# Kernel tuning notes

Hardware: AMD Instinct MI355X
Metric: run time of the kernel (lower is better)

The kernel has to match this reference:

```python
import jax, jax.numpy as jnp
from jax import lax
import numpy as np

B, T = 64, 256
V_CHAR, V_DICT = 8000, 30
CHAR_E, POS_E = 256, 128
POS_H, MAIN_H = 256, 512      # bidirectional output dims
LBL = 18 + 2                  # label_size + START/STOP


def _lstm_dir(x, maskf, Wih, Whh, b):
    """Unidirectional LSTM with PyTorch gate order (i,f,g,o); masked steps hold state, outputs zeroed at pads."""
    Bb = x.shape[0]
    H = Whh.shape[1]
    def step(carry, inp):
        h, c = carry
        xt, mt = inp  # xt [B,D], mt [B,1]
        g = xt @ Wih.T + h @ Whh.T + b
        i, f, gg, o = jnp.split(g, 4, axis=-1)
        c2 = jax.nn.sigmoid(f) * c + jax.nn.sigmoid(i) * jnp.tanh(gg)
        h2 = jax.nn.sigmoid(o) * jnp.tanh(c2)
        h = mt * h2 + (1.0 - mt) * h
        c = mt * c2 + (1.0 - mt) * c
        return (h, c), h * mt
    init = (jnp.zeros((Bb, H), x.dtype), jnp.zeros((Bb, H), x.dtype))
    _, ys = lax.scan(step, init, (x.transpose(1, 0, 2), maskf.T[:, :, None]))
    return ys.transpose(1, 0, 2)  # [B,T,H]


def _bilstm(x, lengths, maskf, Wih_f, Whh_f, b_f, Wih_b, Whh_b, b_b):
    """Packed-sequence BiLSTM: backward direction runs over each sequence reversed by its own length."""
    Tt = x.shape[1]
    out_f = _lstm_dir(x, maskf, Wih_f, Whh_f, b_f)
    rev_idx = jnp.clip(lengths[:, None] - 1 - jnp.arange(Tt)[None, :], 0, Tt - 1)  # [B,T]
    x_rev = jnp.take_along_axis(x, rev_idx[:, :, None], axis=1)
    out_b_rev = _lstm_dir(x_rev, maskf, Wih_b, Whh_b, b_b)
    out_b = jnp.take_along_axis(out_b_rev, rev_idx[:, :, None], axis=1) * maskf[:, :, None]
    return jnp.concatenate([out_f, out_b], axis=-1)


def _viterbi(emit, mask, trans):
    """CRF Viterbi decode. emit [B,T,L], mask [B,T] bool, trans [L,L] (trans[i,j]=score i->j); START=L-2, STOP=L-1."""
    Bb, Tt, L = emit.shape
    START, STOP = L - 2, L - 1
    alpha0 = trans[START][None, :] + emit[:, 0]  # [B,L]
    ident = jnp.arange(L)[None, :]
    def step(alpha, inp):
        e_t, m_t = inp  # [B,L], [B,1]
        scores = alpha[:, :, None] + trans[None, :, :]  # [B,L_prev,L_cur]
        bp = jnp.argmax(scores, axis=1)
        new = jnp.max(scores, axis=1) + e_t
        alpha = jnp.where(m_t, new, alpha)
        bp = jnp.where(m_t, bp, ident)
        return alpha, bp
    alpha, bps = lax.scan(step, alpha0, (emit[:, 1:].transpose(1, 0, 2), mask[:, 1:].T[:, :, None]))
    final = alpha + trans[:, STOP][None, :]
    last_tag = jnp.argmax(final, axis=1)          # [B]
    path_score = jnp.max(final, axis=1)           # [B]
    def back(tag, bp_t):
        prev = jnp.take_along_axis(bp_t, tag[:, None], axis=1)[:, 0]
        return prev, tag
    first_tag, tags_rest = lax.scan(back, last_tag, bps, reverse=True)  # tags_rest [T-1,B]
    tags = jnp.concatenate([first_tag[:, None], tags_rest.T], axis=1)   # [B,T]
    return path_score, tags * mask.astype(tags.dtype)


def setup_inputs() -> dict:
    key = jax.random.key(0)
    ks = jax.random.split(key, 24)
    char_inputs = jax.random.randint(ks[0], (B, T), 0, V_CHAR)
    pos_inputs = jax.random.randint(ks[1], (B, T), 0, V_DICT)
    tag_inputs = jax.random.randint(ks[2], (B, T), 0, V_DICT)
    lengths = jnp.sort(jax.random.randint(ks[3], (B,), T // 2, T + 1))[::-1]
    lengths = lengths.at[0].set(T)  # pack_padded requires descending lengths; max len defines T
    mask = jnp.arange(T)[None, :] < lengths[:, None]
    s = 0.08
    def rn(k, shape):
        return jax.random.normal(k, shape, jnp.float32) * s
    Hp, Hm = POS_H // 2, MAIN_H // 2
    Dm = CHAR_E + POS_E + POS_H
    return dict(
        char_inputs=char_inputs, pos_inputs=pos_inputs, tag_inputs=tag_inputs,
        lengths=lengths, mask=mask,
        char_emb=rn(ks[4], (V_CHAR, CHAR_E)),
        pos_emb=rn(ks[5], (V_DICT, POS_E)),
        tag_pos_emb=rn(ks[6], (V_DICT, POS_E)),
        pWih_f=rn(ks[7], (4 * Hp, POS_E)), pWhh_f=rn(ks[8], (4 * Hp, Hp)), pb_f=rn(ks[9], (4 * Hp,)),
        pWih_b=rn(ks[10], (4 * Hp, POS_E)), pWhh_b=rn(ks[11], (4 * Hp, Hp)), pb_b=rn(ks[12], (4 * Hp,)),
        mWih_f=rn(ks[13], (4 * Hm, Dm)), mWhh_f=rn(ks[14], (4 * Hm, Hm)), mb_f=rn(ks[15], (4 * Hm,)),
        mWih_b=rn(ks[16], (4 * Hm, Dm)), mWhh_b=rn(ks[17], (4 * Hm, Hm)), mb_b=rn(ks[18], (4 * Hm,)),
        W_out=rn(ks[19], (LBL, MAIN_H)), b_out=rn(ks[20], (LBL,)),
        trans=rn(ks[21], (LBL, LBL)),
    )


def reference(char_inputs, pos_inputs, tag_inputs, lengths, mask,
              char_emb, pos_emb, tag_pos_emb,
              pWih_f, pWhh_f, pb_f, pWih_b, pWhh_b, pb_b,
              mWih_f, mWhh_f, mb_f, mWih_b, mWhh_b, mb_b,
              W_out, b_out, trans):
    maskf = mask.astype(jnp.float32)
    # PosBiLSTM: embeds tag_inputs with its own pos table, runs BiLSTM (dropout is identity at eval)
    tag_embs = tag_pos_emb[tag_inputs]
    pos_lstm_out = _bilstm(tag_embs, lengths, maskf, pWih_f, pWhh_f, pb_f, pWih_b, pWhh_b, pb_b)
    # Main BiLSTM over [char_emb | pos_emb | pos_lstm_out]
    emb = jnp.concatenate([char_emb[char_inputs], pos_emb[pos_inputs], pos_lstm_out], axis=-1)
    lstm_out = _bilstm(emb, lengths, maskf, mWih_f, mWhh_f, mb_f, mWih_b, mWhh_b, mb_b)
    emit = lstm_out @ W_out.T + b_out  # [B,T,LBL]
    _, tag_seq = _viterbi(emit, mask, trans)
    return tag_seq
```

## Files before the change

### kernel.cpp

```cpp
#include <hip/hip_runtime.h>
#include <hip/hip_bf16.h>
#include <math.h>


#define Bsz 64
#define Tsz 256
#define NROW 16384

__device__ __forceinline__ float sigm(float x) { return 1.f / (1.f + expf(-x)); }

#define PIN4(v) asm volatile("" : "+v"((v).x), "+v"((v).y), "+v"((v).z), "+v"((v).w))

typedef float f32x4 __attribute__((ext_vector_type(4)));
typedef short short8 __attribute__((ext_vector_type(8)));
typedef unsigned short u16;
typedef u16 u16x8 __attribute__((ext_vector_type(8)));

__device__ __forceinline__ void bf16split(float f, u16& h, u16& l) {
  unsigned u = __float_as_uint(f);
  unsigned hh = (u + 0x7FFFu + ((u >> 16) & 1u)) >> 16;
  h = (u16)hh;
  float hf = __uint_as_float(hh << 16);
  unsigned v = __float_as_uint(f - hf);
  l = (u16)((v + 0x7FFFu + ((v >> 16) & 1u)) >> 16);
}

__global__ __launch_bounds__(256) void wsplit4(
    const float* __restrict__ s0, u16* __restrict__ h0, u16* __restrict__ l0, int n0,
    const float* __restrict__ s1, u16* __restrict__ h1, u16* __restrict__ l1, int n1,
    const float* __restrict__ s2, u16* __restrict__ h2, u16* __restrict__ l2, int n2,
    const float* __restrict__ s3, u16* __restrict__ h3, u16* __restrict__ l3, int n3) {
  int i = (blockIdx.x * 256 + threadIdx.x) * 4;
  const float* s; u16 *h, *l;
  if (i < n0) { s = s0; h = h0; l = l0; }
  else if ((i -= n0) < n1) { s = s1; h = h1; l = l1; }
  else if ((i -= n1) < n2) { s = s2; h = h2; l = l2; }
  else if ((i -= n2) < n3) { s = s3; h = h3; l = l3; }
  else return;
  float4 v = *(const float4*)&s[i];
  ushort4 hh, ll;
  bf16split(v.x, hh.x, ll.x); bf16split(v.y, hh.y, ll.y);
  bf16split(v.z, hh.z, ll.z); bf16split(v.w, hh.w, ll.w);
  *(ushort4*)&h[i] = hh; *(ushort4*)&l[i] = ll;
}

__global__ __launch_bounds__(256) void gather_kernel(
    const int* __restrict__ ci, const int* __restrict__ pi, const int* __restrict__ ti,
    const float* __restrict__ ce, const float* __restrict__ pe, const float* __restrict__ te,
    u16* __restrict__ tbh, u16* __restrict__ tbl,
    u16* __restrict__ emh, u16* __restrict__ eml) {
  int gid = blockIdx.x * 256 + threadIdx.x;
  int m = gid >> 7, s = gid & 127;
  float4 v; size_t off; u16 *ph, *pl;
  if (s < 32) {
    v = ((const float4*)&te[(size_t)ti[m] * 128])[s];
    off = (size_t)m * 128 + s * 4; ph = tbh; pl = tbl;
  } else if (s < 96) {
    v = ((const float4*)&ce[(size_t)ci[m] * 256])[s - 32];
    off = (size_t)m * 640 + (s - 32) * 4; ph = emh; pl = eml;
  } else {
    v = ((const float4*)&pe[(size_t)pi[m] * 128])[s - 96];
    off = (size_t)m * 640 + 256 + (s - 96) * 4; ph = emh; pl = eml;
  }
  ushort4 h, l;
  bf16split(v.x, h.x, l.x); bf16split(v.y, h.y, l.y);
  bf16split(v.z, h.z, l.z); bf16split(v.w, h.w, l.w);
  *(ushort4*)&ph[off] = h; *(ushort4*)&pl[off] = l;
}

#define GTM 512
#define GTN 128
__global__ __launch_bounds__(512) void gemm_bf16x3(
    const u16* __restrict__ Ah, const u16* __restrict__ Al,
    const u16* __restrict__ Wh, const u16* __restrict__ Wl,
    const float* __restrict__ biasF, const float* __restrict__ biasB,
    float* __restrict__ C, int ldc, int K, int NhB) {
  extern __shared__ u16 us[];
  u16* As_h = us;
  u16* As_l = us + 512 * 40;
  u16* Ws_h = us + 2 * 512 * 40;
  u16* Ws_l = us + 2 * 512 * 40 + 128 * 40;
  const int tid = threadIdx.x;
  const int lane = tid & 63, wv = tid >> 6;
  const int l15 = lane & 15, l8 = (lane >> 4) * 8, l4 = lane >> 4;
  const int m0 = blockIdx.y * GTM;
  const int n0 = blockIdx.x * GTN;
  const u16* WhS = Wh + (size_t)n0 * K;
  const u16* WlS = Wl + (size_t)n0 * K;
  const float* bias = (blockIdx.x < (unsigned)NhB) ? (biasF + n0)
                                                   : (biasB + (n0 - NhB * GTN));
  const int arow = tid >> 2, aq = (tid & 3) * 8;

  u16x8 rA[4][2], rW[2];
#define LOAD_TILES(k0)                                                         \
  {                                                                            \
    _Pragma("unroll")                                                          \
    for (int r = 0; r < 4; ++r) {                                              \
      int row = arow + r * 128;                                                \
      rA[r][0] = *(const u16x8*)&Ah[(size_t)(m0 + row) * K + (k0) + aq];       \
      rA[r][1] = *(const u16x8*)&Al[(size_t)(m0 + row) * K + (k0) + aq];       \
    }                                                                          \
    rW[0] = *(const u16x8*)&WhS[(size_t)arow * K + (k0) + aq];                 \
    rW[1] = *(const u16x8*)&WlS[(size_t)arow * K + (k0) + aq];                 \
  }

  f32x4 acc[4][8] = {};
  LOAD_TILES(0);
  for (int k0 = 0; k0 < K; k0 += 32) {
#pragma unroll
    for (int r = 0; r < 4; ++r) {
      int row = arow + r * 128;
      *(u16x8*)&As_h[row * 40 + aq] = rA[r][0];
      *(u16x8*)&As_l[row * 40 + aq] = rA[r][1];
    }
    if (arow < 128) {
      *(u16x8*)&Ws_h[arow * 40 + aq] = rW[0];
      *(u16x8*)&Ws_l[arow * 40 + aq] = rW[1];
    }
    __syncthreads();
    if (k0 + 32 < K) LOAD_TILES(k0 + 32);
    short8 aH[4], aL[4];
#pragma unroll
    for (int fr = 0; fr < 4; ++fr) {
      aH[fr] = *(const short8*)&As_h[(wv * 64 + fr * 16 + l15) * 40 + l8];
      aL[fr] = *(const short8*)&As_l[(wv * 64 + fr * 16 + l15) * 40 + l8];
    }
#pragma unroll
    for (int cf = 0; cf < 8; ++cf) {
      short8 bH = *(const short8*)&Ws_h[(cf * 16 + l15) * 40 + l8];
      short8 bL = *(const short8*)&Ws_l[(cf * 16 + l15) * 40 + l8];
#pragma unroll
      for (int fr = 0; fr < 4; ++fr) {
        acc[fr][cf] = __builtin_amdgcn_mfma_f32_16x16x32_bf16(aH[fr], bH, acc[fr][cf], 0, 0, 0);
        acc[fr][cf] = __builtin_amdgcn_mfma_f32_16x16x32_bf16(aH[fr], bL, acc[fr][cf], 0, 0, 0);
        acc[fr][cf] = __builtin_amdgcn_mfma_f32_16x16x32_bf16(aL[fr], bH, acc[fr][cf], 0, 0, 0);
      }
    }
    __syncthreads();
  }
#pragma unroll
  for (int fr = 0; fr < 4; ++fr)
#pragma unroll
    for (int cf = 0; cf < 8; ++cf) {
      int col = cf * 16 + l15;
      float bs = bias[col];
#pragma unroll
      for (int q = 0; q < 4; ++q) {
        size_t row = m0 + wv * 64 + fr * 16 + l4 * 4 + q;
        C[row * ldc + n0 + col] = acc[fr][cf][q] + bs;
      }
    }
#undef LOAD_TILES
}

__global__ __launch_bounds__(512, 2) void pos_rec(
    const int* __restrict__ lengths, const float* __restrict__ gpos,
    const float* __restrict__ Wf, const float* __restrict__ Wb,
    u16* __restrict__ emh, u16* __restrict__ eml) {
  const int blk = blockIdx.x;
  const int b = blk >> 1, dir = blk & 1;
  const int j = threadIdx.x;
  const int gc = j >> 7;
  const int len = lengths[b];
  const float* W = dir ? Wb : Wf;
  __shared__ __align__(16) float h[128];
  __shared__ float gbuf[512];
  float4 w4[32];
#pragma unroll
  for (int i = 0; i < 32; ++i) w4[i] = *(const float4*)&W[(size_t)j * 128 + i * 4];
#pragma unroll
  for (int i = 0; i < 32; ++i) PIN4(w4[i]);
  float c = 0.f;
  if (j < 128) h[j] = 0.f;
  __syncthreads();
  int idx0 = dir ? (len - 1) : 0;
  float gcur = gpos[((size_t)(b * Tsz + idx0)) * 1024 + dir * 512 + j];
  for (int t = 0; t < len; ++t) {
    const int idx = dir ? (len - 1 - t) : t;
    const int tn = (t + 1 < len) ? t + 1 : t;
    const int idxn = dir ? (len - 1 - tn) : tn;
    float gnext = gpos[((size_t)(b * Tsz + idxn)) * 1024 + dir * 512 + j];
    float acc = gcur;
    const float4* h4 = (const float4*)h;
#pragma unroll
    for (int i = 0; i < 32; ++i) {
      float4 hh = h4[i];
      acc = fmaf(hh.x, w4[i].x, acc); acc = fmaf(hh.y, w4[i].y, acc);
      acc = fmaf(hh.z, w4[i].z, acc); acc = fmaf(hh.w, w4[i].w, acc);
    }
    gbuf[j] = (gc == 2) ? tanhf(acc) : sigm(acc);
    __syncthreads();
    if (j < 128) {
      float si = gbuf[j], sf = gbuf[128 + j], tg = gbuf[256 + j], so = gbuf[384 + j];
      c = sf * c + si * tg;
      float hn = so * tanhf(c);
      h[j] = hn;
      u16 hh2, hl2; bf16split(hn, hh2, hl2);
      size_t eo = ((size_t)(b * Tsz + idx)) * 640 + 384 + dir * 128 + j;
      emh[eo] = hh2; eml[eo] = hl2;
    }
    __syncthreads();
    gcur = gnext;
  }
}

#define MR_VF4 40
#define MR_LF4 19
#define MR_TF4 5
#define HX_STRIDE 256
__global__ __launch_bounds__(512, 2) void main_rec(
    const int* __restrict__ lengths, const float* __restrict__ gmain,
    const float* __restrict__ Wf, const float* __restrict__ Wb,
    float* __restrict__ lstm_out, unsigned long long* __restrict__ hx) {
  extern __shared__ float smem[];
  float4* wl  = (float4*)smem;
  float* hbuf = smem + MR_LF4 * 512 * 4;
  float* gbuf = hbuf + 256;

  const int blk = blockIdx.x;
  const int b = blk >> 2, dir = (blk >> 1) & 1, half = blk & 1;
  const int j = threadIdx.x;
  const int gc = j >> 7, ul = j & 127;
  const int r = gc * 256 + half * 128 + ul;
  const int len = lengths[b];
  const float* Wr = (dir ? Wb : Wf) + (size_t)r * 256;

  float4 wv[MR_VF4];
#pragma unroll
  for (int i = 0; i < MR_VF4; ++i) wv[i] = *(const float4*)&Wr[i * 4];
#pragma unroll
  for (int i = 0; i < MR_VF4; ++i) PIN4(wv[i]);
#pragma unroll
  for (int i = 0; i < MR_LF4; ++i) wl[i * 512 + j] = *(const float4*)&Wr[(MR_VF4 + i) * 4];

  unsigned long long* selfD = hx + (size_t)blk * HX_STRIDE;
  unsigned long long* partD = hx + (size_t)(blk ^ 1) * HX_STRIDE;
  const int obase = dir * 256 + half * 128;

  float c = 0.f;
  if (j < 256) hbuf[j] = 0.f;
  __syncthreads();

  const int idx0 = dir ? (len - 1) : 0;
  float gcur = gmain[((size_t)(b * Tsz + idx0)) * 2048 + dir * 1024 + r];
  for (int t = 0; t < len; ++t) {
    const int idx = dir ? (len - 1 - t) : t;
    const int tn = (t + 1 < len) ? t + 1 : t;
    const int idxn = dir ? (len - 1 - tn) : tn;
    float gnext = gmain[((size_t)(b * Tsz + idxn)) * 2048 + dir * 1024 + r];
    float acc = gcur;
    const float4* hb4 = (const float4*)hbuf;
#pragma unroll
    for (int i = 0; i < MR_VF4; ++i) {
      float4 hh = hb4[i], w = wv[i];
      acc = fmaf(hh.x, w.x, acc); acc = fmaf(hh.y, w.y, acc);
      acc = fmaf(hh.z, w.z, acc); acc = fmaf(hh.w, w.w, acc);
    }
#pragma unroll
    for (int i = 0; i < MR_LF4; ++i) {
      float4 hh = hb4[MR_VF4 + i], w = wl[i * 512 + j];
      acc = fmaf(hh.x, w.x, acc); acc = fmaf(hh.y, w.y, acc);
      acc = fmaf(hh.z, w.z, acc); acc = fmaf(hh.w, w.w, acc);
    }
#pragma unroll
    for (int i = 0; i < MR_TF4; ++i) {
      float4 hh = hb4[MR_VF4 + MR_LF4 + i];
      float4 w = *(const float4*)&Wr[(MR_VF4 + MR_LF4 + i) * 4];
      acc = fmaf(hh.x, w.x, acc); acc = fmaf(hh.y, w.y, acc);
      acc = fmaf(hh.z, w.z, acc); acc = fmaf(hh.w, w.w, acc);
    }
    gbuf[j] = (gc == 2) ? tanhf(acc) : sigm(acc);
    __syncthreads();
    if (j < 128) {
      float si = gbuf[ul], sf = gbuf[128 + ul], tg = gbuf[256 + ul], so = gbuf[384 + ul];
      c = sf * c + si * tg;
      float hn = so * tanhf(c);
      if (t + 1 < len) {
        union { float f; unsigned u; } cv; cv.f = hn;
        unsigned long long pk =
            ((unsigned long long)(unsigned)(t + 1) << 32) | (unsigned long long)cv.u;
        __hip_atomic_store(&selfD[(t & 1) * 128 + ul], pk,
                           __ATOMIC_RELAXED, __HIP_MEMORY_SCOPE_AGENT);
      }
      lstm_out[((size_t)(b * Tsz + idx)) * 512 + obase + ul] = hn;
      hbuf[half * 128 + ul] = hn;
      if (t + 1 < len) {
        unsigned long long pv; int guard = 0;
        for (;;) {
          pv = __hip_atomic_load(&partD[(t & 1) * 128 + ul],
                                 __ATOMIC_RELAXED, __HIP_MEMORY_SCOPE_AGENT);
          if ((unsigned)(pv >> 32) == (unsigned)(t + 1)) break;
          if (++guard > (1 << 22)) break;
          __builtin_amdgcn_s_sleep(1);
        }
        union { unsigned u; float f; } hv; hv.u = (unsigned)(pv & 0xffffffffull);
        hbuf[(half ^ 1) * 128 + ul] = hv.f;
      }
    }
    __syncthreads();
    gcur = gnext;
  }
}

__global__ __launch_bounds__(256) void emit_kernel(
    const float* __restrict__ lstm_out, const float* __restrict__ Wout,
    const float* __restrict__ bout, float* __restrict__ emit) {
  int gid = blockIdx.x * 256 + threadIdx.x;
  int m = gid >> 5, j = gid & 31;
  if (j >= 20) return;
  const float4* xr = (const float4*)&lstm_out[(size_t)m * 512];
  const float4* wr = (const float4*)&Wout[(size_t)j * 512];
  float acc = bout[j];
#pragma unroll 8
  for (int i = 0; i < 128; ++i) {
    float4 x = xr[i], w = wr[i];
    acc += x.x * w.x + x.y * w.y + x.z * w.z + x.w * w.w;
  }
  emit[(size_t)m * 20 + j] = acc;
}

__global__ __launch_bounds__(64) void viterbi_kernel(
    const int* __restrict__ lengths, const float* __restrict__ emit,
    const float* __restrict__ trans, int* __restrict__ out) {
  const int b = blockIdx.x, j = threadIdx.x;
  const int len = lengths[b];
  __shared__ float tr[400];
  __shared__ float alpha[20];
  __shared__ float fin[20];
  __shared__ unsigned char bp[256][20];
  for (int i = j; i < 400; i += 64) tr[i] = trans[i];
  __syncthreads();
  if (j < 20) alpha[j] = tr[18 * 20 + j] + emit[(size_t)(b * Tsz) * 20 + j];
  __syncthreads();
  for (int t = 1; t < len; ++t) {
    float best = 0.f; int bi = 0;
    if (j < 20) {
      best = alpha[0] + tr[j];
#pragma unroll
      for (int i = 1; i < 20; ++i) {
        float s = alpha[i] + tr[i * 20 + j];
        if (s > best) { best = s; bi = i; }
      }
      best += emit[((size_t)(b * Tsz + t)) * 20 + j];
    }
    __syncthreads();
    if (j < 20) { alpha[j] = best; bp[t][j] = (unsigned char)bi; }
    __syncthreads();
  }
  if (j < 20) fin[j] = alpha[j] + tr[j * 20 + 19];
  __syncthreads();
  if (j == 0) {
    float best = fin[0]; int tag = 0;
    for (int i = 1; i < 20; ++i) if (fin[i] > best) { best = fin[i]; tag = i; }
    out[b * Tsz + len - 1] = tag;
    for (int t = len - 1; t >= 1; --t) { tag = bp[t][tag]; out[b * Tsz + t - 1] = tag; }
  }
  for (int t = len + j; t < Tsz; t += 64) out[b * Tsz + t] = 0;
}

extern "C" void kernel_launch(void* const* d_in, const int* in_sizes, int n_in,
                              void* d_out, int out_size, void* d_ws, size_t ws_size,
                              hipStream_t stream) {
  const int*   char_in = (const int*)d_in[0];
  const int*   pos_in  = (const int*)d_in[1];
  const int*   tag_in  = (const int*)d_in[2];
  const int*   lengths = (const int*)d_in[3];
  const float* ce      = (const float*)d_in[5];
  const float* pe      = (const float*)d_in[6];
  const float* te      = (const float*)d_in[7];
  const float* pWih_f  = (const float*)d_in[8];
  const float* pWhh_f  = (const float*)d_in[9];
  const float* pb_f    = (const float*)d_in[10];
  const float* pWih_b  = (const float*)d_in[11];
  const float* pWhh_b  = (const float*)d_in[12];
  const float* pb_b    = (const float*)d_in[13];
  const float* mWih_f  = (const float*)d_in[14];
  const float* mWhh_f  = (const float*)d_in[15];
  const float* mb_f    = (const float*)d_in[16];
  const float* mWih_b  = (const float*)d_in[17];
  const float* mWhh_b  = (const float*)d_in[18];
  const float* mb_b    = (const float*)d_in[19];
  const float* W_out   = (const float*)d_in[20];
  const float* b_out   = (const float*)d_in[21];
  const float* trans   = (const float*)d_in[22];

  float* ws = (float*)d_ws;
  const size_t WPH     = 0;
  const size_t WPL     = 65536;
  const size_t WMH     = 131072;
  const size_t WML     = 786432;
  const size_t EMH     = 1441792;
  const size_t EML     = 6684672;
  const size_t TBH     = 11927552;
  const size_t TBL     = 12976128;
  const size_t GPOS    = 14024704;
  const size_t GMAIN   = 11927552;
  const size_t LSTMOUT = 1441792;
  const size_t EMIT    = 9830400;
  const size_t HX      = 45481984;

  hipMemsetAsync(ws + HX, 0, HX_STRIDE * 256 * sizeof(unsigned long long), stream);

  wsplit4<<<1408, 256, 0, stream>>>(
      pWih_f, (u16*)(ws + WPH),          (u16*)(ws + WPL),          65536,
      pWih_b, (u16*)(ws + WPH) + 65536,  (u16*)(ws + WPL) + 65536,  65536,
      mWih_f, (u16*)(ws + WMH),          (u16*)(ws + WML),          655360,
      mWih_b, (u16*)(ws + WMH) + 655360, (u16*)(ws + WML) + 655360, 655360);

  gather_kernel<<<8192, 256, 0, stream>>>(char_in, pos_in, tag_in, ce, pe, te,
                                          (u16*)(ws + TBH), (u16*)(ws + TBL),
                                          (u16*)(ws + EMH), (u16*)(ws + EML));

  const int GSMEM = (2 * 512 * 40 + 2 * 128 * 40) * 2;
  hipFuncSetAttribute((const void*)gemm_bf16x3,
                      hipFuncAttributeMaxDynamicSharedMemorySize, GSMEM);

  gemm_bf16x3<<<dim3(8, 32), 512, GSMEM, stream>>>(
      (u16*)(ws + TBH), (u16*)(ws + TBL),
      (u16*)(ws + WPH), (u16*)(ws + WPL),
      pb_f, pb_b, ws + GPOS, 1024, 128, 4);

  pos_rec<<<128, 512, 0, stream>>>(lengths, ws + GPOS, pWhh_f, pWhh_b,
                                   (u16*)(ws + EMH), (u16*)(ws + EML));

  gemm_bf16x3<<<dim3(16, 32), 512, GSMEM, stream>>>(
      (u16*)(ws + EMH), (u16*)(ws + EML),
      (u16*)(ws + WMH), (u16*)(ws + WML),
      mb_f, mb_b, ws + GMAIN, 2048, 640, 8);

  const int SMEM = MR_LF4 * 512 * 16 + 256 * 4 + 512 * 4;
  hipFuncSetAttribute((const void*)main_rec,
                      hipFuncAttributeMaxDynamicSharedMemorySize, SMEM);
  main_rec<<<256, 512, SMEM, stream>>>(lengths, ws + GMAIN, mWhh_f, mWhh_b,
                                       ws + LSTMOUT, (unsigned long long*)(ws + HX));

  emit_kernel<<<2048, 256, 0, stream>>>(ws + LSTMOUT, W_out, b_out, ws + EMIT);

  viterbi_kernel<<<64, 64, 0, stream>>>(lengths, ws + EMIT, trans, (int*)d_out);
}
```

Measured before the change: 1.266 ms.

## Overlap own-half recurrent matvec with partner hidden-state exchange wait

```diff
diff --git a/kernel.cpp b/kernel.cpp
--- a/kernel.cpp
+++ b/kernel.cpp
@@ -204,18 +204,20 @@
   }
 }
 
-#define MR_VF4 40
-#define MR_LF4 19
-#define MR_TF4 5
+#define MR_OWN 32
+#define MR_PV  8
+#define MR_PL  19
+#define MR_PT  5
 #define HX_STRIDE 256
 __global__ __launch_bounds__(512, 2) void main_rec(
     const int* __restrict__ lengths, const float* __restrict__ gmain,
     const float* __restrict__ Wf, const float* __restrict__ Wb,
     float* __restrict__ lstm_out, unsigned long long* __restrict__ hx) {
   extern __shared__ float smem[];
-  float4* wl  = (float4*)smem;
-  float* hbuf = smem + MR_LF4 * 512 * 4;
-  float* gbuf = hbuf + 256;
+  float4* wl   = (float4*)smem;
+  float* hown  = smem + MR_PL * 512 * 4;
+  float* hpart = hown + 128;
+  float* gbuf  = hpart + 128;
 
   const int blk = blockIdx.x;
   const int b = blk >> 2, dir = (blk >> 1) & 1, half = blk & 1;
@@ -224,53 +226,32 @@
   const int r = gc * 256 + half * 128 + ul;
   const int len = lengths[b];
   const float* Wr = (dir ? Wb : Wf) + (size_t)r * 256;
-
-  float4 wv[MR_VF4];
-#pragma unroll
-  for (int i = 0; i < MR_VF4; ++i) wv[i] = *(const float4*)&Wr[i * 4];
-#pragma unroll
-  for (int i = 0; i < MR_VF4; ++i) PIN4(wv[i]);
-#pragma unroll
-  for (int i = 0; i < MR_LF4; ++i) wl[i * 512 + j] = *(const float4*)&Wr[(MR_VF4 + i) * 4];
+  const int ob = half * 128, pb = (half ^ 1) * 128;
+
+  float4 wv[MR_OWN + MR_PV];
+#pragma unroll
+  for (int i = 0; i < MR_OWN; ++i) wv[i] = *(const float4*)&Wr[ob + i * 4];
+#pragma unroll
+  for (int i = 0; i < MR_PV; ++i) wv[MR_OWN + i] = *(const float4*)&Wr[pb + i * 4];
+#pragma unroll
+  for (int i = 0; i < MR_OWN + MR_PV; ++i) PIN4(wv[i]);
+#pragma unroll
+  for (int i = 0; i < MR_PL; ++i) wl[i * 512 + j] = *(const float4*)&Wr[pb + 32 + i * 4];
 
   unsigned long long* selfD = hx + (size_t)blk * HX_STRIDE;
   unsigned long long* partD = hx + (size_t)(blk ^ 1) * HX_STRIDE;
   const int obase = dir * 256 + half * 128;
 
+  const int idx0 = dir ? (len - 1) : 0;
+  float g0 = gmain[((size_t)(b * Tsz + idx0)) * 2048 + dir * 1024 + r];
+  gbuf[j] = (gc == 2) ? tanhf(g0) : sigm(g0);
+  const int idx1 = dir ? (len - 2) : 1;
+  float gnext = gmain[((size_t)(b * Tsz + idx1)) * 2048 + dir * 1024 + r];
   float c = 0.f;
-  if (j < 256) hbuf[j] = 0.f;
   __syncthreads();
 
-  const int idx0 = dir ? (len - 1) : 0;
-  float gcur = gmain[((size_t)(b * Tsz + idx0)) * 2048 + dir * 1024 + r];
   for (int t = 0; t < len; ++t) {
     const int idx = dir ? (len - 1 - t) : t;
-    const int tn = (t + 1 < len) ? t + 1 : t;
-    const int idxn = dir ? (len - 1 - tn) : tn;
-    float gnext = gmain[((size_t)(b * Tsz + idxn)) * 2048 + dir * 1024 + r];
-    float acc = gcur;
-    const float4* hb4 = (const float4*)hbuf;
-#pragma unroll
-    for (int i = 0; i < MR_VF4; ++i) {
-      float4 hh = hb4[i], w = wv[i];
-      acc = fmaf(hh.x, w.x, acc); acc = fmaf(hh.y, w.y, acc);
-      acc = fmaf(hh.z, w.z, acc); acc = fmaf(hh.w, w.w, acc);
-    }
-#pragma unroll
-    for (int i = 0; i < MR_LF4; ++i) {
-      float4 hh = hb4[MR_VF4 + i], w = wl[i * 512 + j];
-      acc = fmaf(hh.x, w.x, acc); acc = fmaf(hh.y, w.y, acc);
-      acc = fmaf(hh.z, w.z, acc); acc = fmaf(hh.w, w.w, acc);
-    }
-#pragma unroll
-    for (int i = 0; i < MR_TF4; ++i) {
-      float4 hh = hb4[MR_VF4 + MR_LF4 + i];
-      float4 w = *(const float4*)&Wr[(MR_VF4 + MR_LF4 + i) * 4];
-      acc = fmaf(hh.x, w.x, acc); acc = fmaf(hh.y, w.y, acc);
-      acc = fmaf(hh.z, w.z, acc); acc = fmaf(hh.w, w.w, acc);
-    }
-    gbuf[j] = (gc == 2) ? tanhf(acc) : sigm(acc);
-    __syncthreads();
     if (j < 128) {
       float si = gbuf[ul], sf = gbuf[128 + ul], tg = gbuf[256 + ul], so = gbuf[384 + ul];
       c = sf * c + si * tg;
@@ -283,22 +264,64 @@
                            __ATOMIC_RELAXED, __HIP_MEMORY_SCOPE_AGENT);
       }
       lstm_out[((size_t)(b * Tsz + idx)) * 512 + obase + ul] = hn;
-      hbuf[half * 128 + ul] = hn;
-      if (t + 1 < len) {
-        unsigned long long pv; int guard = 0;
-        for (;;) {
-          pv = __hip_atomic_load(&partD[(t & 1) * 128 + ul],
-                                 __ATOMIC_RELAXED, __HIP_MEMORY_SCOPE_AGENT);
-          if ((unsigned)(pv >> 32) == (unsigned)(t + 1)) break;
-          if (++guard > (1 << 22)) break;
-          __builtin_amdgcn_s_sleep(1);
-        }
-        union { unsigned u; float f; } hv; hv.u = (unsigned)(pv & 0xffffffffull);
-        hbuf[(half ^ 1) * 128 + ul] = hv.f;
-      }
-    }
-    __syncthreads();
-    gcur = gnext;
+      hown[ul] = hn;
+    }
+    if (t + 1 == len) break;
+    __syncthreads();
+
+    float acc = gnext;
+    {
+      const float4* ho = (const float4*)hown;
+#pragma unroll
+      for (int i = 0; i < MR_OWN; ++i) {
+        float4 hh = ho[i], w = wv[i];
+        acc = fmaf(hh.x, w.x, acc); acc = fmaf(hh.y, w.y, acc);
+        acc = fmaf(hh.z, w.z, acc); acc = fmaf(hh.w, w.w, acc);
+      }
+    }
+    const int t2 = (t + 2 < len) ? t + 2 : len - 1;
+    const int idx2 = dir ? (len - 1 - t2) : t2;
+    float gnn = gmain[((size_t)(b * Tsz + idx2)) * 2048 + dir * 1024 + r];
+
+    if (j < 128) {
+      unsigned long long pv; int guard = 0;
+      for (;;) {
+        pv = __hip_atomic_load(&partD[(t & 1) * 128 + ul],
+                               __ATOMIC_RELAXED, __HIP_MEMORY_SCOPE_AGENT);
+        if ((unsigned)(pv >> 32) == (unsigned)(t + 1)) break;
+        if (++guard > (1 << 22)) break;
+        __builtin_amdgcn_s_sleep(1);
+      }
+      union { unsigned u; float f; } hv; hv.u = (unsigned)(pv & 0xffffffffull);
+      hpart[ul] = hv.f;
+    }
+    __syncthreads();
+
+    {
+      const float4* hp = (const float4*)hpart;
+#pragma unroll
+      for (int i = 0; i < MR_PV; ++i) {
+        float4 hh = hp[i], w = wv[MR_OWN + i];
+        acc = fmaf(hh.x, w.x, acc); acc = fmaf(hh.y, w.y, acc);
+        acc = fmaf(hh.z, w.z, acc); acc = fmaf(hh.w, w.w, acc);
+      }
+#pragma unroll
+      for (int i = 0; i < MR_PL; ++i) {
+        float4 hh = hp[MR_PV + i], w = wl[i * 512 + j];
+        acc = fmaf(hh.x, w.x, acc); acc = fmaf(hh.y, w.y, acc);
+        acc = fmaf(hh.z, w.z, acc); acc = fmaf(hh.w, w.w, acc);
+      }
+#pragma unroll
+      for (int i = 0; i < MR_PT; ++i) {
+        float4 hh = hp[MR_PV + MR_PL + i];
+        float4 w = *(const float4*)&Wr[pb + 108 + i * 4];
+        acc = fmaf(hh.x, w.x, acc); acc = fmaf(hh.y, w.y, acc);
+        acc = fmaf(hh.z, w.z, acc); acc = fmaf(hh.w, w.w, acc);
+      }
+    }
+    gbuf[j] = (gc == 2) ? tanhf(acc) : sigm(acc);
+    __syncthreads();
+    gnext = gnn;
   }
 }
 
@@ -428,7 +451,7 @@
       (u16*)(ws + WMH), (u16*)(ws + WML),
       mb_f, mb_b, ws + GMAIN, 2048, 640, 8);
 
-  const int SMEM = MR_LF4 * 512 * 16 + 256 * 4 + 512 * 4;
+  const int SMEM = MR_PL * 512 * 16 + 128 * 4 + 128 * 4 + 512 * 4;
   hipFuncSetAttribute((const void*)main_rec,
                       hipFuncAttributeMaxDynamicSharedMemorySize, SMEM);
   main_rec<<<256, 512, SMEM, stream>>>(lengths, ws + GMAIN, mWhh_f, mWhh_b,
```

Measured after the change: 4.228 ms. 234% more time.
